# Kernel tuning notes

Measured on AMD Instinct MI355X. Metric: run time of the kernel, lower is better.

The kernel has to match this reference:

```python
import jax, jax.numpy as jnp
import numpy as np

B, C, H, W = 4, 256, 64, 64
GROUPS = 32
EPS = 1e-6
N_BITS_QKV = 8
N_BITS_SM = 8


def setup_inputs() -> dict:
    key = jax.random.key(0)
    ks = jax.random.split(key, 6)
    s = 1.0 / np.sqrt(C)
    return {
        "x": jax.random.normal(ks[0], (B, C, H, W), jnp.float32),
        "gn_scale": jnp.ones((C,), jnp.float32),
        "gn_bias": jnp.zeros((C,), jnp.float32),
        "wq": jax.random.normal(ks[1], (C, C), jnp.float32) * s,
        "bq": jnp.zeros((C,), jnp.float32),
        "wk": jax.random.normal(ks[2], (C, C), jnp.float32) * s,
        "bk": jnp.zeros((C,), jnp.float32),
        "wv": jax.random.normal(ks[3], (C, C), jnp.float32) * s,
        "bv": jnp.zeros((C,), jnp.float32),
        "wproj": jax.random.normal(ks[4], (C, C), jnp.float32) * s,
        "bproj": jnp.zeros((C,), jnp.float32),
        # per-tensor uniform-affine quantizer params (delta, zero_point)
        "dq": jnp.float32(8.0 / 255.0), "zq": jnp.float32(128.0),
        "dk": jnp.float32(8.0 / 255.0), "zk": jnp.float32(128.0),
        "dv": jnp.float32(8.0 / 255.0), "zv": jnp.float32(128.0),
        "dw": jnp.float32(1.0 / 255.0), "zw": jnp.float32(0.0),
    }


def ste_round(x):
    # round with straight-through gradient (as in round_ste of BRECQ/QDrop)
    return x + jax.lax.stop_gradient(jnp.round(x) - x)


def fake_quant(x, delta, zero_point, n_bits):
    # UniformAffineQuantizer: quant -> clamp -> dequant
    n_levels = 2 ** n_bits
    x_int = ste_round(x / delta) + zero_point
    x_q = jnp.clip(x_int, 0, n_levels - 1)
    return (x_q - zero_point) * delta


def group_norm(x, scale, bias):
    b, c, h, w = x.shape
    xg = x.reshape(b, GROUPS, (c // GROUPS) * h * w)
    mu = xg.mean(-1, keepdims=True)
    var = xg.var(-1, keepdims=True)
    xn = ((xg - mu) * jax.lax.rsqrt(var + EPS)).reshape(b, c, h, w)
    return xn * scale[None, :, None, None] + bias[None, :, None, None]


def conv1x1(x, w, b):
    # 1x1 conv == channel-mixing matmul
    return jnp.einsum('bchw,oc->bohw', x, w) + b[None, :, None, None]


def reference(x, gn_scale, gn_bias, wq, bq, wk, bk, wv, bv, wproj, bproj,
              dq, zq, dk, zk, dv, zv, dw, zw):
    h_ = group_norm(x, gn_scale, gn_bias)
    q = conv1x1(h_, wq, bq)
    k = conv1x1(h_, wk, bk)
    v = conv1x1(h_, wv, bv)
    b, c, h, w = q.shape
    hw = h * w
    q = q.reshape(b, c, hw).transpose(0, 2, 1)   # [b, hw, c]
    k = k.reshape(b, c, hw)                      # [b, c, hw]
    q = fake_quant(q, dq, zq, N_BITS_QKV)
    k = fake_quant(k, dk, zk, N_BITS_QKV)
    attn = jnp.einsum('bnc,bcm->bnm', q, k) * (c ** -0.5)  # [b, hw, hw]
    attn = jax.nn.softmax(attn, axis=2)
    v = fake_quant(v.reshape(b, c, hw), dv, zv, N_BITS_QKV)
    attn = fake_quant(attn.transpose(0, 2, 1), dw, zw, N_BITS_SM)  # [b, m, n]
    h_out = jnp.einsum('bcm,bmn->bcn', v, attn).reshape(b, c, h, w)
    return x + conv1x1(h_out, wproj, bproj)
```

## Files before the change

kernel.cpp:

```cpp
#include <hip/hip_runtime.h>


#define Bb 4
#define Cc 256
#define Nn 4096
#define NGRP 32
#define LOG2E 1.4426950408889634f

typedef unsigned short u16;
typedef unsigned int   u32;
typedef unsigned char  u8;
typedef __attribute__((ext_vector_type(8))) short bf16x8;
typedef __attribute__((ext_vector_type(4))) float f32x4;
typedef __attribute__((ext_vector_type(4))) int   i32x4;

#define MFMA16(a,b,c)    __builtin_amdgcn_mfma_f32_16x16x32_bf16((a),(b),(c),0,0,0)
#define MFMA_I8(a,b,c)   __builtin_amdgcn_mfma_i32_16x16x64_i8((a),(b),(c),0,0,0)
#define EXP2F(x)         __builtin_amdgcn_exp2f(x)

static __device__ __forceinline__ u16 f2bf(float x){
  u32 u = __float_as_uint(x);
  u += 0x7fffu + ((u >> 16) & 1u);
  return (u16)(u >> 16);
}
static __device__ __forceinline__ float bf2f(u16 h){ return __uint_as_float(((u32)h) << 16); }

union U64c { u16 u[4]; uint2 v; };

__global__ __launch_bounds__(256) void k_gn_stats(const float* __restrict__ x,
                                                  float* __restrict__ mu, float* __restrict__ rs){
  int bg = blockIdx.x;
  const float4* p = (const float4*)(x + (size_t)bg * (8 * Nn));
  float s = 0.f, q = 0.f;
  for (int i = threadIdx.x; i < 8*Nn/4; i += 256){
    float4 v = p[i];
    s += v.x + v.y + v.z + v.w;
    q += v.x*v.x + v.y*v.y + v.z*v.z + v.w*v.w;
  }
  __shared__ float rsum[256], rsq[256];
  rsum[threadIdx.x] = s; rsq[threadIdx.x] = q;
  __syncthreads();
  for (int off = 128; off > 0; off >>= 1){
    if (threadIdx.x < off){ rsum[threadIdx.x] += rsum[threadIdx.x+off]; rsq[threadIdx.x] += rsq[threadIdx.x+off]; }
    __syncthreads();
  }
  if (threadIdx.x == 0){
    const float inv = 1.0f / (8*Nn);
    float m = rsum[0]*inv;
    float var = rsq[0]*inv - m*m;
    mu[bg] = m; rs[bg] = rsqrtf(var + 1e-6f);
  }
}

__global__ __launch_bounds__(256) void k_wsplit(const float* __restrict__ wq, const float* __restrict__ wk,
                                                const float* __restrict__ wv, const float* __restrict__ wp,
                                                u16* __restrict__ WH, u16* __restrict__ WL){
  int gid = blockIdx.x*256 + threadIdx.x;
  int mat = gid >> 16, idx = gid & 65535;
  const float* src = (mat == 0) ? wq : (mat == 1) ? wk : (mat == 2) ? wv : wp;
  float w = src[idx];
  u16 h = f2bf(w);
  WH[gid] = h;
  WL[gid] = f2bf(w - bf2f(h));
}

__global__ __launch_bounds__(256) void k_gn_apply(const float* __restrict__ x,
                                                  const float* __restrict__ gsc, const float* __restrict__ gbi,
                                                  const float* __restrict__ mu, const float* __restrict__ rs,
                                                  u16* __restrict__ hhi, u16* __restrict__ hlo){
  int nt = blockIdx.x, ct = blockIdx.y, b = blockIdx.z;
  int n0 = nt*64, c0 = ct*64;
  __shared__ float yt[64*65];
  __shared__ float sa[64], sb[64];
  int t = threadIdx.x;
  if (t < 64){
    int c = c0 + t;
    int bg = b*NGRP + (c >> 3);
    float a = rs[bg] * gsc[c];
    sa[t] = a;
    sb[t] = gbi[c] - mu[bg]*a;
  }
  __syncthreads();
  #pragma unroll
  for (int j = 0; j < 4; ++j){
    int id = t + j*256;
    int r = id >> 4, cq = id & 15;
    float4 v = *(const float4*)(x + ((size_t)b*Cc + c0 + r)*Nn + n0 + cq*4);
    float a = sa[r], bb = sb[r];
    yt[r*65 + cq*4 + 0] = v.x*a + bb;
    yt[r*65 + cq*4 + 1] = v.y*a + bb;
    yt[r*65 + cq*4 + 2] = v.z*a + bb;
    yt[r*65 + cq*4 + 3] = v.w*a + bb;
  }
  __syncthreads();
  int nl = t >> 2, cg = (t & 3) * 16;
  size_t base = ((size_t)b*Nn + n0 + nl)*Cc + c0 + cg;
  #pragma unroll
  for (int half = 0; half < 2; ++half){
    union { u16 u[8]; uint4 v; } Ph, Pl;
    #pragma unroll
    for (int u = 0; u < 8; ++u){
      float y = yt[(cg + half*8 + u)*65 + nl];
      u16 h = f2bf(y);
      Ph.u[u] = h; Pl.u[u] = f2bf(y - bf2f(h));
    }
    *(uint4*)(hhi + base + half*8) = Ph.v;
    *(uint4*)(hlo + base + half*8) = Pl.v;
  }
}

__global__ __launch_bounds__(1024) void k_convqkv(const u16* __restrict__ WH, const u16* __restrict__ WL,
                                                 const u16* __restrict__ Hhi, const u16* __restrict__ Hlo,
                                                 const float* __restrict__ bq, const float* __restrict__ bk,
                                                 const float* __restrict__ bv,
                                                 const float* __restrict__ dq, const float* __restrict__ zq,
                                                 const float* __restrict__ dk, const float* __restrict__ zk,
                                                 const float* __restrict__ dv, const float* __restrict__ zv,
                                                 u8* __restrict__ qT8, u8* __restrict__ kT8,
                                                 u8* __restrict__ v8){
  int nt = blockIdx.x, b = blockIdx.y;
  __shared__ u16 Lh[64*256], Ll[64*256];
  int t = threadIdx.x, lane = t & 63, wave = t >> 6;
  int lo16 = lane & 15, quad = lane >> 4;
  int o0 = wave*16;

  {
    const u16* hb = Hhi + ((size_t)b*Nn + nt*64) * 256;
    const u16* lb = Hlo + ((size_t)b*Nn + nt*64) * 256;
    #pragma unroll
    for (int j = 0; j < 2; ++j){
      int id = t + j*1024;
      int r = id >> 5, ch = id & 31;
      int sw = (ch ^ (r & 15)) * 8;
      *(uint4*)(Lh + r*256 + sw) = *(const uint4*)(hb + (size_t)r*256 + ch*8);
      *(uint4*)(Ll + r*256 + sw) = *(const uint4*)(lb + (size_t)r*256 + ch*8);
    }
  }
  __syncthreads();

  const float* Bs[3] = {bq, bk, bv};
  const float* Dsr[3] = {dq, dk, dv};
  const float* Zs[3] = {zq, zk, zv};

  #pragma unroll
  for (int ws = 0; ws < 3; ++ws){
    bf16x8 awh[8], awl[8];
    {
      const u16* wbh = WH + (size_t)ws*65536 + (size_t)(o0 + lo16) * 256 + quad*8;
      const u16* wbl = WL + (size_t)ws*65536 + (size_t)(o0 + lo16) * 256 + quad*8;
      #pragma unroll
      for (int k = 0; k < 8; ++k){
        awh[k] = *(const bf16x8*)(wbh + k*32);
        awl[k] = *(const bf16x8*)(wbl + k*32);
      }
    }
    f32x4 zf = {0.f,0.f,0.f,0.f};
    f32x4 acc[4] = {zf, zf, zf, zf};
    #pragma unroll
    for (int k = 0; k < 8; ++k){
      #pragma unroll
      for (int ns = 0; ns < 4; ++ns){
        int r = ns*16 + lo16;
        int ph = ((k*4 + quad) ^ (r & 15)) * 8;
        bf16x8 bh = *(const bf16x8*)(Lh + r*256 + ph);
        bf16x8 bl = *(const bf16x8*)(Ll + r*256 + ph);
        acc[ns] = MFMA16(awh[k], bh, acc[ns]);
        acc[ns] = MFMA16(awl[k], bh, acc[ns]);
        acc[ns] = MFMA16(awh[k], bl, acc[ns]);
      }
    }
    float bia[4];
    #pragma unroll
    for (int r = 0; r < 4; ++r) bia[r] = Bs[ws][o0 + quad*4 + r];
    float z = Zs[ws][0]; float invd = 1.0f / Dsr[ws][0];

    if (ws < 2){
      u8* outT = (ws == 0) ? qT8 : kT8;
      #pragma unroll
      for (int ns = 0; ns < 4; ++ns){
        int n = nt*64 + ns*16 + lo16;
        u32 w = 0;
        #pragma unroll
        for (int r = 0; r < 4; ++r){
          float v = acc[ns][r] + bia[r];
          float xq = fminf(fmaxf(rintf(v*invd) + z, 0.f), 255.f);
          int qi = (int)rintf(xq - z);
          w |= ((u32)(qi & 255)) << (8*r);
        }
        *(u32*)(outT + ((size_t)b*Nn + n)*Cc + o0 + quad*4) = w;
      }
    } else {
      #pragma unroll
      for (int ns = 0; ns < 4; ++ns){
        int n = nt*64 + ns*16 + lo16;
        #pragma unroll
        for (int r = 0; r < 4; ++r){
          float v = acc[ns][r] + bia[r];
          float xq = fminf(fmaxf(rintf(v*invd) + z, 0.f), 255.f);
          int qi = (int)rintf(xq - z);
          v8[((size_t)b*Cc + o0 + quad*4 + r)*Nn + n] = (u8)(qi & 255);
        }
      }
    }
  }
}

static __device__ __forceinline__ int sq4(u32 w){
  int s = 0;
  #pragma unroll
  for (int j = 0; j < 4; ++j){ int v = (int)((signed char)((w >> (8*j)) & 0xffu)); s += v*v; }
  return s;
}
static __device__ __forceinline__ int ssum4(u32 w){
  return ((int)(w << 24) >> 24) + ((int)(w << 16) >> 24) + ((int)(w << 8) >> 24) + ((int)w >> 24);
}
__global__ __launch_bounds__(256) void k_normvs(const u8* __restrict__ qT8, const u8* __restrict__ kT8,
                                                const u8* __restrict__ v8,
                                                u32* __restrict__ stat, int* __restrict__ vsum){
  if (blockIdx.x < 128){
    int gid = blockIdx.x*256 + threadIdx.x;
    int which = gid >> 14;
    int rid = gid & 16383;
    const u8* row = (which ? kT8 : qT8) + (size_t)rid * 256;
    u32 acc = 0;
    const uint4* p = (const uint4*)row;
    #pragma unroll
    for (int i = 0; i < 16; ++i){
      uint4 w = p[i];
      acc += (u32)(sq4(w.x) + sq4(w.y) + sq4(w.z) + sq4(w.w));
    }
    #pragma unroll
    for (int msk = 32; msk > 0; msk >>= 1){
      u32 o = (u32)__shfl_xor((int)acc, msk, 64);
      acc = acc > o ? acc : o;
    }
    if ((threadIdx.x & 63) == 0)
      atomicMax(&stat[which*4 + (rid >> 12)], acc);
  } else {
    int row = blockIdx.x - 128;
    uint4 w = *(const uint4*)(v8 + (size_t)row*Nn + threadIdx.x*16);
    int s = ssum4(w.x) + ssum4(w.y) + ssum4(w.z) + ssum4(w.w);
    #pragma unroll
    for (int msk = 1; msk < 64; msk <<= 1) s += __shfl_xor(s, msk, 64);
    __shared__ int r4[4];
    if ((threadIdx.x & 63) == 0) r4[threadIdx.x >> 6] = s;
    __syncthreads();
    if (threadIdx.x == 0) vsum[row] = r4[0] + r4[1] + r4[2] + r4[3];
  }
}

__global__ __launch_bounds__(1024) void k_qpv(const u8* __restrict__ qT8, const u8* __restrict__ kT8,
                                              const u8* __restrict__ v8,
                                              const u32* __restrict__ stat,
                                              const float* __restrict__ pdq, const float* __restrict__ pdk,
                                              const float* __restrict__ pdw, const float* __restrict__ pzw,
                                              const int* __restrict__ vsum,
                                              const float* __restrict__ pdv,
                                              const u16* __restrict__ WH, const u16* __restrict__ WL,
                                              const float* __restrict__ bp,
                                              const float* __restrict__ xres,
                                              float* __restrict__ outF){
  int nt = blockIdx.x, b = blockIdx.y;
  __shared__ alignas(16) u8  Kt[2][2][64*256];
  __shared__ alignas(16) u32 Pt[2][2][64*16];
  __shared__ float Lbuf[4][4][16];
  int t = threadIdx.x, lane = t & 63, w = t >> 6;
  int lo16 = lane & 15, q = lane >> 4;
  int ms = w & 3, nsq = w >> 2;

  float sc2 = pdq[0]*pdk[0]*0.0625f*LOG2E;
  float M2 = sc2 * sqrtf((float)stat[b] * (float)stat[4+b]);
  float zw = pzw[0];

  i32x4 qf[4];
  {
    const u8* qb = qT8 + ((size_t)b*Nn + nt*64 + nsq*16 + lo16)*256;
    #pragma unroll
    for (int kk = 0; kk < 4; ++kk)
      qf[kk] = *(const i32x4*)(qb + kk*64 + q*16);
  }

  int krow = t >> 4, kch = t & 15;
  int kdst = krow*256 + ((kch ^ (krow & 15)) << 4);
  const u8* kb = kT8 + (size_t)b*Nn*256;

  int mrow = ms*16 + lo16;
  int kofs[4];
  #pragma unroll
  for (int kk = 0; kk < 4; ++kk) kofs[kk] = mrow*256 + (((kk*4 + q) ^ (mrow & 15)) << 4);

  const u8* vp = v8 + ((size_t)(b*Cc + w*16 + lo16))*Nn + q*16;

  float lr = 0.f;
  {
    const u8* kld = kb + (size_t)krow*256 + kch*16;
    uint4 kr0 = *(const uint4*)(kld);
    uint4 kr1 = *(const uint4*)(kld + 16384);
    *(uint4*)(Kt[0][0] + kdst) = kr0;
    *(uint4*)(Kt[0][1] + kdst) = kr1;
    kld += 2*16384;
    kr0 = *(const uint4*)(kld);
    kr1 = *(const uint4*)(kld + 16384);
    kld += 2*16384;
    __syncthreads();
    i32x4 spA0, spB0, spA1, spB1;
    #pragma unroll 2
    for (int i = 0; i < 32; ++i){
      int cur = i & 1;
      i32x4 sA0 = {0,0,0,0}, sB0 = {0,0,0,0}, sA1 = {0,0,0,0}, sB1 = {0,0,0,0};
      sA0 = MFMA_I8(*(const i32x4*)(Kt[cur][0] + kofs[0]), qf[0], sA0);
      sB0 = MFMA_I8(*(const i32x4*)(Kt[cur][0] + kofs[1]), qf[1], sB0);
      sA1 = MFMA_I8(*(const i32x4*)(Kt[cur][1] + kofs[0]), qf[0], sA1);
      sB1 = MFMA_I8(*(const i32x4*)(Kt[cur][1] + kofs[1]), qf[1], sB1);
      sA0 = MFMA_I8(*(const i32x4*)(Kt[cur][0] + kofs[2]), qf[2], sA0);
      sB0 = MFMA_I8(*(const i32x4*)(Kt[cur][0] + kofs[3]), qf[3], sB0);
      sA1 = MFMA_I8(*(const i32x4*)(Kt[cur][1] + kofs[2]), qf[2], sA1);
      sB1 = MFMA_I8(*(const i32x4*)(Kt[cur][1] + kofs[3]), qf[3], sB1);
      if (i < 31){
        *(uint4*)(Kt[cur ^ 1][0] + kdst) = kr0;
        *(uint4*)(Kt[cur ^ 1][1] + kdst) = kr1;
        if (i < 30){
          kr0 = *(const uint4*)(kld);
          kr1 = *(const uint4*)(kld + 16384);
          kld += 2*16384;
        }
      }
      if (i > 0){
        #pragma unroll
        for (int r = 0; r < 4; ++r){
          lr += EXP2F(fmaf((float)(spA0[r] + spB0[r]), sc2, -M2));
          lr += EXP2F(fmaf((float)(spA1[r] + spB1[r]), sc2, -M2));
        }
      }
      spA0 = sA0; spB0 = sB0; spA1 = sA1; spB1 = sB1;
      __syncthreads();
    }
    #pragma unroll
    for (int r = 0; r < 4; ++r){
      lr += EXP2F(fmaf((float)(spA0[r] + spB0[r]), sc2, -M2));
      lr += EXP2F(fmaf((float)(spA1[r] + spB1[r]), sc2, -M2));
    }
  }
  lr += __shfl_xor(lr, 16, 64);
  lr += __shfl_xor(lr, 32, 64);
  if (lane < 16) Lbuf[nsq][ms][lo16] = lr;
  __syncthreads();
  float Ls = Lbuf[nsq][0][lo16] + Lbuf[nsq][1][lo16] + Lbuf[nsq][2][lo16] + Lbuf[nsq][3][lo16];
  float crn = __log2f(1.0f / (pdw[0] * Ls)) - M2;

  i32x4 zi = {0,0,0,0};
  i32x4 acc[4] = {zi,zi,zi,zi};
  int nrow = nsq*16 + lo16;
  int pdst = nrow*16 + ((ms ^ (nrow & 3) ^ ((nrow >> 2) & 3)) << 2) + q;
  int pofs[4];
  #pragma unroll
  for (int ns = 0; ns < 4; ++ns){
    int pr = ns*16 + lo16;
    pofs[ns] = pr*16 + ((q ^ (pr & 3) ^ ((pr >> 2) & 3)) << 2);
  }
  {
    const u8* kld = kb + (size_t)krow*256 + kch*16;
    uint4 kr0 = *(const uint4*)(kld);
    uint4 kr1 = *(const uint4*)(kld + 16384);
    *(uint4*)(Kt[0][0] + kdst) = kr0;
    *(uint4*)(Kt[0][1] + kdst) = kr1;
    kld += 2*16384;
    kr0 = *(const uint4*)(kld);
    kr1 = *(const uint4*)(kld + 16384);
    kld += 2*16384;
    const u8* vld = vp + 128;
    i32x4 af0 = *(const i32x4*)(vp);
    i32x4 af1 = *(const i32x4*)(vp + 64);
    i32x4 af0p, af1p, af0pp, af1pp;
    i32x4 spA0, spB0, spA1, spB1;
    __syncthreads();
    #pragma unroll 2
    for (int i = 0; i < 32; ++i){
      int cur = i & 1;
      i32x4 sA0 = {0,0,0,0}, sB0 = {0,0,0,0}, sA1 = {0,0,0,0}, sB1 = {0,0,0,0};
      sA0 = MFMA_I8(*(const i32x4*)(Kt[cur][0] + kofs[0]), qf[0], sA0);
      sB0 = MFMA_I8(*(const i32x4*)(Kt[cur][0] + kofs[1]), qf[1], sB0);
      sA1 = MFMA_I8(*(const i32x4*)(Kt[cur][1] + kofs[0]), qf[0], sA1);
      sB1 = MFMA_I8(*(const i32x4*)(Kt[cur][1] + kofs[1]), qf[1], sB1);
      sA0 = MFMA_I8(*(const i32x4*)(Kt[cur][0] + kofs[2]), qf[2], sA0);
      sB0 = MFMA_I8(*(const i32x4*)(Kt[cur][0] + kofs[3]), qf[3], sB0);
      sA1 = MFMA_I8(*(const i32x4*)(Kt[cur][1] + kofs[2]), qf[2], sA1);
      sB1 = MFMA_I8(*(const i32x4*)(Kt[cur][1] + kofs[3]), qf[3], sB1);
      if (i < 31){
        *(uint4*)(Kt[cur ^ 1][0] + kdst) = kr0;
        *(uint4*)(Kt[cur ^ 1][1] + kdst) = kr1;
        if (i < 30){
          kr0 = *(const uint4*)(kld);
          kr1 = *(const uint4*)(kld + 16384);
          kld += 2*16384;
        }
      }
      if (i > 1){
        acc[0] = MFMA_I8(af0pp, *(const i32x4*)(Pt[cur][0] + pofs[0]), acc[0]);
        acc[1] = MFMA_I8(af0pp, *(const i32x4*)(Pt[cur][0] + pofs[1]), acc[1]);
        acc[2] = MFMA_I8(af0pp, *(const i32x4*)(Pt[cur][0] + pofs[2]), acc[2]);
        acc[3] = MFMA_I8(af0pp, *(const i32x4*)(Pt[cur][0] + pofs[3]), acc[3]);
        acc[0] = MFMA_I8(af1pp, *(const i32x4*)(Pt[cur][1] + pofs[0]), acc[0]);
        acc[1] = MFMA_I8(af1pp, *(const i32x4*)(Pt[cur][1] + pofs[1]), acc[1]);
        acc[2] = MFMA_I8(af1pp, *(const i32x4*)(Pt[cur][1] + pofs[2]), acc[2]);
        acc[3] = MFMA_I8(af1pp, *(const i32x4*)(Pt[cur][1] + pofs[3]), acc[3]);
      }
      if (i > 0){
        u32 wp0 = 0, wp1 = 0;
        #pragma unroll
        for (int r = 0; r < 4; ++r){
          float at0 = EXP2F(fmaf((float)(spA0[r] + spB0[r]), sc2, crn));
          float y0 = fminf(fmaxf(rintf(at0) + zw, 0.f), 255.f);
          wp0 = __builtin_amdgcn_cvt_pk_u8_f32(y0, (u32)r, wp0);
          float at1 = EXP2F(fmaf((float)(spA1[r] + spB1[r]), sc2, crn));
          float y1 = fminf(fmaxf(rintf(at1) + zw, 0.f), 255.f);
          wp1 = __builtin_amdgcn_cvt_pk_u8_f32(y1, (u32)r, wp1);
        }
        Pt[cur ^ 1][0][pdst] = wp0 ^ 0x80808080u;
        Pt[cur ^ 1][1][pdst] = wp1 ^ 0x80808080u;
      }
      spA0 = sA0; spB0 = sB0; spA1 = sA1; spB1 = sB1;
      af0pp = af0p; af0p = af0; af1pp = af1p; af1p = af1;
      if (i < 31){
        af0 = *(const i32x4*)(vld);
        af1 = *(const i32x4*)(vld + 64);
        vld += 128;
      }
      __syncthreads();
    }
    acc[0] = MFMA_I8(af0pp, *(const i32x4*)(Pt[0][0] + pofs[0]), acc[0]);
    acc[1] = MFMA_I8(af0pp, *(const i32x4*)(Pt[0][0] + pofs[1]), acc[1]);
    acc[2] = MFMA_I8(af0pp, *(const i32x4*)(Pt[0][0] + pofs[2]), acc[2]);
    acc[3] = MFMA_I8(af0pp, *(const i32x4*)(Pt[0][0] + pofs[3]), acc[3]);
    acc[0] = MFMA_I8(af1pp, *(const i32x4*)(Pt[0][1] + pofs[0]), acc[0]);
    acc[1] = MFMA_I8(af1pp, *(const i32x4*)(Pt[0][1] + pofs[1]), acc[1]);
    acc[2] = MFMA_I8(af1pp, *(const i32x4*)(Pt[0][1] + pofs[2]), acc[2]);
    acc[3] = MFMA_I8(af1pp, *(const i32x4*)(Pt[0][1] + pofs[3]), acc[3]);
    {
      u32 wp0 = 0, wp1 = 0;
      #pragma unroll
      for (int r = 0; r < 4; ++r){
        float at0 = EXP2F(fmaf((float)(spA0[r] + spB0[r]), sc2, crn));
        float y0 = fminf(fmaxf(rintf(at0) + zw, 0.f), 255.f);
        wp0 = __builtin_amdgcn_cvt_pk_u8_f32(y0, (u32)r, wp0);
        float at1 = EXP2F(fmaf((float)(spA1[r] + spB1[r]), sc2, crn));
        float y1 = fminf(fmaxf(rintf(at1) + zw, 0.f), 255.f);
        wp1 = __builtin_amdgcn_cvt_pk_u8_f32(y1, (u32)r, wp1);
      }
      Pt[1][0][pdst] = wp0 ^ 0x80808080u;
      Pt[1][1][pdst] = wp1 ^ 0x80808080u;
    }
    __syncthreads();
    acc[0] = MFMA_I8(af0p, *(const i32x4*)(Pt[1][0] + pofs[0]), acc[0]);
    acc[1] = MFMA_I8(af0p, *(const i32x4*)(Pt[1][0] + pofs[1]), acc[1]);
    acc[2] = MFMA_I8(af0p, *(const i32x4*)(Pt[1][0] + pofs[2]), acc[2]);
    acc[3] = MFMA_I8(af0p, *(const i32x4*)(Pt[1][0] + pofs[3]), acc[3]);
    acc[0] = MFMA_I8(af1p, *(const i32x4*)(Pt[1][1] + pofs[0]), acc[0]);
    acc[1] = MFMA_I8(af1p, *(const i32x4*)(Pt[1][1] + pofs[1]), acc[1]);
    acc[2] = MFMA_I8(af1p, *(const i32x4*)(Pt[1][1] + pofs[2]), acc[2]);
    acc[3] = MFMA_I8(af1p, *(const i32x4*)(Pt[1][1] + pofs[3]), acc[3]);
  }

  u16* Ht = (u16*)Kt;
  {
    float s = pdv[0] * pdw[0];
    float corr = s * (128.0f - zw);
    int c0 = w*16 + q*4;
    int kc0 = c0 >> 7;
    int ch8 = (c0 >> 3) & 15;
    int c4  = c0 & 7;
    float cv[4];
    #pragma unroll
    for (int r = 0; r < 4; ++r) cv[r] = corr * (float)vsum[b*Cc + c0 + r];
    #pragma unroll
    for (int ns = 0; ns < 4; ++ns){
      int rrow = ns*16 + lo16;
      U64c Uh;
      #pragma unroll
      for (int r = 0; r < 4; ++r)
        Uh.u[r] = f2bf(s*(float)acc[ns][r] + cv[r]);
      *(uint2*)(Ht + rrow*256 + kc0*128 + ((ch8 ^ (rrow & 7)) << 3) + c4) = Uh.v;
    }
  }
  __syncthreads();
  {
    f32x4 zf = {0.f,0.f,0.f,0.f};
    f32x4 acc2[4] = {zf, zf, zf, zf};
    const u16* wbh = WH + (size_t)3*65536 + (size_t)(w*16 + lo16)*256 + q*8;
    const u16* wbl = WL + (size_t)3*65536 + (size_t)(w*16 + lo16)*256 + q*8;
    #pragma unroll
    for (int kc = 0; kc < 2; ++kc){
      bf16x8 ah[4], al[4];
      #pragma unroll
      for (int k4 = 0; k4 < 4; ++k4){
        ah[k4] = *(const bf16x8*)(wbh + kc*128 + k4*32);
        al[k4] = *(const bf16x8*)(wbl + kc*128 + k4*32);
      }
      #pragma unroll
      for (int k4 = 0; k4 < 4; ++k4){
        #pragma unroll
        for (int ns = 0; ns < 4; ++ns){
          int rrow = ns*16 + lo16;
          bf16x8 bh = *(const bf16x8*)(Ht + rrow*256 + kc*128 + (((k4*4 + q) ^ (rrow & 7)) << 3));
          acc2[ns] = MFMA16(ah[k4], bh, acc2[ns]);
          acc2[ns] = MFMA16(al[k4], bh, acc2[ns]);
        }
      }
    }
    float bia[4];
    #pragma unroll
    for (int r = 0; r < 4; ++r) bia[r] = bp[w*16 + q*4 + r];
    #pragma unroll
    for (int ns = 0; ns < 4; ++ns){
      int n = nt*64 + ns*16 + lo16;
      #pragma unroll
      for (int r = 0; r < 4; ++r){
        size_t a = ((size_t)b*Cc + w*16 + q*4 + r)*Nn + n;
        outF[a] = xres[a] + acc2[ns][r] + bia[r];
      }
    }
  }
}

extern "C" void kernel_launch(void* const* d_in, const int* in_sizes, int n_in,
                              void* d_out, int out_size, void* d_ws, size_t ws_size,
                              hipStream_t stream){
  (void)in_sizes; (void)n_in; (void)out_size; (void)ws_size;
  const float* x   = (const float*)d_in[0];
  const float* gsc = (const float*)d_in[1];
  const float* gbi = (const float*)d_in[2];
  const float* wq  = (const float*)d_in[3];
  const float* bq  = (const float*)d_in[4];
  const float* wk  = (const float*)d_in[5];
  const float* bk  = (const float*)d_in[6];
  const float* wv  = (const float*)d_in[7];
  const float* bv  = (const float*)d_in[8];
  const float* wp  = (const float*)d_in[9];
  const float* bp  = (const float*)d_in[10];
  const float* dq  = (const float*)d_in[11];
  const float* zq  = (const float*)d_in[12];
  const float* dk  = (const float*)d_in[13];
  const float* zk  = (const float*)d_in[14];
  const float* dv  = (const float*)d_in[15];
  const float* zv  = (const float*)d_in[16];
  const float* dw  = (const float*)d_in[17];
  const float* zw  = (const float*)d_in[18];
  float* out = (float*)d_out;

  const size_t SZT = (size_t)Bb*Nn*Cc;
  u16* hT_hi = (u16*)d_ws;
  u16* hT_lo = hT_hi + SZT;
  u16* h2    = hT_lo + SZT;
  u8*  qT8   = (u8*)(h2 + SZT);
  u8*  kT8   = qT8 + SZT;
  u8*  v8    = kT8 + SZT;
  u16* WH    = (u16*)(v8 + SZT);
  u16* WL    = WH + 4*65536;
  float* mu  = (float*)(WL + 4*65536);
  float* rs  = mu + 128;
  u32*  stat = (u32*)(rs + 128);
  int*  vsum = (int*)(stat + 8);

  k_gn_stats<<<dim3(Bb*NGRP), 256, 0, stream>>>(x, mu, rs);
  k_wsplit<<<dim3(1024), 256, 0, stream>>>(wq, wk, wv, wp, WH, WL);
  k_gn_apply<<<dim3(Nn/64, Cc/64, Bb), 256, 0, stream>>>(x, gsc, gbi, mu, rs, hT_hi, hT_lo);

  k_convqkv<<<dim3(Nn/64, Bb), 1024, 0, stream>>>(WH, WL, hT_hi, hT_lo,
                                                  bq, bk, bv, dq, zq, dk, zk, dv, zv,
                                                  qT8, kT8, v8);

  hipMemsetAsync(stat, 0, 8*sizeof(u32), stream);
  k_normvs<<<dim3(128 + Bb*Cc), 256, 0, stream>>>(qT8, kT8, v8, stat, vsum);

  k_qpv<<<dim3(Nn/64, Bb), 1024, 0, stream>>>(qT8, kT8, v8, stat, dq, dk, dw, zw, vsum, dv,
                                              WH, WL, bp, x, out);
}
```

Before: 244.3 us.

## Fuse group-norm apply and norm/vsum statistics into QKV conv kernel

The group-norm application moves into the QKV 1x1-conv kernel. Each block now reads x directly, normalizes it, splits it into bf16 hi/lo parts and writes those into swizzled LDS, so the hT_hi/hT_lo global intermediates are no longer written and read back. The per-row squared-norm max statistics for q/k and the per-channel v sums are computed in the conv epilogue through LDS and global atomics, which removes the separate k_normvs pass that re-read the int8 outputs. In exchange the conv kernel needs more LDS and extra barriers in a serialized four-step staging loop, and it adds atomic contention.

```diff
diff --git a/kernel.cpp b/kernel.cpp
--- a/kernel.cpp
+++ b/kernel.cpp
@@ -64,79 +64,66 @@
   WL[gid] = f2bf(w - bf2f(h));
 }
 
-__global__ __launch_bounds__(256) void k_gn_apply(const float* __restrict__ x,
-                                                  const float* __restrict__ gsc, const float* __restrict__ gbi,
-                                                  const float* __restrict__ mu, const float* __restrict__ rs,
-                                                  u16* __restrict__ hhi, u16* __restrict__ hlo){
-  int nt = blockIdx.x, ct = blockIdx.y, b = blockIdx.z;
-  int n0 = nt*64, c0 = ct*64;
-  __shared__ float yt[64*65];
-  __shared__ float sa[64], sb[64];
-  int t = threadIdx.x;
-  if (t < 64){
-    int c = c0 + t;
-    int bg = b*NGRP + (c >> 3);
-    float a = rs[bg] * gsc[c];
-    sa[t] = a;
-    sb[t] = gbi[c] - mu[bg]*a;
-  }
-  __syncthreads();
-  #pragma unroll
-  for (int j = 0; j < 4; ++j){
-    int id = t + j*256;
-    int r = id >> 4, cq = id & 15;
-    float4 v = *(const float4*)(x + ((size_t)b*Cc + c0 + r)*Nn + n0 + cq*4);
-    float a = sa[r], bb = sb[r];
-    yt[r*65 + cq*4 + 0] = v.x*a + bb;
-    yt[r*65 + cq*4 + 1] = v.y*a + bb;
-    yt[r*65 + cq*4 + 2] = v.z*a + bb;
-    yt[r*65 + cq*4 + 3] = v.w*a + bb;
-  }
-  __syncthreads();
-  int nl = t >> 2, cg = (t & 3) * 16;
-  size_t base = ((size_t)b*Nn + n0 + nl)*Cc + c0 + cg;
-  #pragma unroll
-  for (int half = 0; half < 2; ++half){
-    union { u16 u[8]; uint4 v; } Ph, Pl;
-    #pragma unroll
-    for (int u = 0; u < 8; ++u){
-      float y = yt[(cg + half*8 + u)*65 + nl];
-      u16 h = f2bf(y);
-      Ph.u[u] = h; Pl.u[u] = f2bf(y - bf2f(h));
-    }
-    *(uint4*)(hhi + base + half*8) = Ph.v;
-    *(uint4*)(hlo + base + half*8) = Pl.v;
-  }
-}
-
-__global__ __launch_bounds__(1024) void k_convqkv(const u16* __restrict__ WH, const u16* __restrict__ WL,
-                                                 const u16* __restrict__ Hhi, const u16* __restrict__ Hlo,
+__global__ __launch_bounds__(1024) void k_convqkv(const float* __restrict__ x,
+                                                 const float* __restrict__ gsc, const float* __restrict__ gbi,
+                                                 const float* __restrict__ mu, const float* __restrict__ rs,
+                                                 const u16* __restrict__ WH, const u16* __restrict__ WL,
                                                  const float* __restrict__ bq, const float* __restrict__ bk,
                                                  const float* __restrict__ bv,
                                                  const float* __restrict__ dq, const float* __restrict__ zq,
                                                  const float* __restrict__ dk, const float* __restrict__ zk,
                                                  const float* __restrict__ dv, const float* __restrict__ zv,
                                                  u8* __restrict__ qT8, u8* __restrict__ kT8,
-                                                 u8* __restrict__ v8){
+                                                 u8* __restrict__ v8,
+                                                 u32* __restrict__ stat, int* __restrict__ vsum){
   int nt = blockIdx.x, b = blockIdx.y;
   __shared__ u16 Lh[64*256], Ll[64*256];
+  __shared__ float yt[64*65];
+  __shared__ float sa[256], sb[256];
+  __shared__ u32 rowacc[2][64];
   int t = threadIdx.x, lane = t & 63, wave = t >> 6;
   int lo16 = lane & 15, quad = lane >> 4;
   int o0 = wave*16;
+  int n0 = nt*64;
+
+  if (t < 256){
+    int c = t;
+    int bg = b*NGRP + (c >> 3);
+    float a = rs[bg] * gsc[c];
+    sa[c] = a;
+    sb[c] = gbi[c] - mu[bg]*a;
+  }
+  if (t < 128) rowacc[t >> 6][t & 63] = 0;
+  __syncthreads();
 
   {
-    const u16* hb = Hhi + ((size_t)b*Nn + nt*64) * 256;
-    const u16* lb = Hlo + ((size_t)b*Nn + nt*64) * 256;
-    #pragma unroll
-    for (int j = 0; j < 2; ++j){
-      int id = t + j*1024;
-      int r = id >> 5, ch = id & 31;
-      int sw = (ch ^ (r & 15)) * 8;
-      *(uint4*)(Lh + r*256 + sw) = *(const uint4*)(hb + (size_t)r*256 + ch*8);
-      *(uint4*)(Ll + r*256 + sw) = *(const uint4*)(lb + (size_t)r*256 + ch*8);
-    }
-  }
-  __syncthreads();
+    int r  = t >> 4, cq = t & 15;
+    int nl = t >> 4, c4 = t & 15;
+    #pragma unroll
+    for (int ct = 0; ct < 4; ++ct){
+      int c0 = ct*64;
+      float4 xv = *(const float4*)(x + ((size_t)b*Cc + c0 + r)*Nn + n0 + cq*4);
+      float a = sa[c0 + r], bb = sb[c0 + r];
+      yt[r*65 + cq*4 + 0] = xv.x*a + bb;
+      yt[r*65 + cq*4 + 1] = xv.y*a + bb;
+      yt[r*65 + cq*4 + 2] = xv.z*a + bb;
+      yt[r*65 + cq*4 + 3] = xv.w*a + bb;
+      __syncthreads();
+      int cg = c0 + c4*4;
+      union { u16 us[4]; uint2 v2; } Ph, Pl;
+      #pragma unroll
+      for (int uu = 0; uu < 4; ++uu){
+        float y = yt[(c4*4 + uu)*65 + nl];
+        u16 h = f2bf(y);
+        Ph.us[uu] = h; Pl.us[uu] = f2bf(y - bf2f(h));
+      }
+      int ch = cg >> 3;
+      int addr = nl*256 + ((ch ^ (nl & 15)) << 3) + (cg & 7);
+      *(uint2*)(Lh + addr) = Ph.v2;
+      *(uint2*)(Ll + addr) = Pl.v2;
+      __syncthreads();
+    }
+  }
 
   const float* Bs[3] = {bq, bk, bv};
   const float* Dsr[3] = {dq, dk, dv};
@@ -179,17 +166,23 @@
       #pragma unroll
       for (int ns = 0; ns < 4; ++ns){
         int n = nt*64 + ns*16 + lo16;
-        u32 w = 0;
+        u32 wpk = 0;
+        int nrm = 0;
         #pragma unroll
         for (int r = 0; r < 4; ++r){
           float v = acc[ns][r] + bia[r];
           float xq = fminf(fmaxf(rintf(v*invd) + z, 0.f), 255.f);
           int qi = (int)rintf(xq - z);
-          w |= ((u32)(qi & 255)) << (8*r);
-        }
-        *(u32*)(outT + ((size_t)b*Nn + n)*Cc + o0 + quad*4) = w;
+          nrm += qi*qi;
+          wpk |= ((u32)(qi & 255)) << (8*r);
+        }
+        *(u32*)(outT + ((size_t)b*Nn + n)*Cc + o0 + quad*4) = wpk;
+        nrm += __shfl_xor(nrm, 16, 64);
+        nrm += __shfl_xor(nrm, 32, 64);
+        if (lane < 16) atomicAdd(&rowacc[ws][ns*16 + lo16], (u32)nrm);
       }
     } else {
+      int vpart[4] = {0, 0, 0, 0};
       #pragma unroll
       for (int ns = 0; ns < 4; ++ns){
         int n = nt*64 + ns*16 + lo16;
@@ -198,54 +191,33 @@
           float v = acc[ns][r] + bia[r];
           float xq = fminf(fmaxf(rintf(v*invd) + z, 0.f), 255.f);
           int qi = (int)rintf(xq - z);
+          vpart[r] += qi;
           v8[((size_t)b*Cc + o0 + quad*4 + r)*Nn + n] = (u8)(qi & 255);
         }
       }
-    }
-  }
-}
-
-static __device__ __forceinline__ int sq4(u32 w){
-  int s = 0;
-  #pragma unroll
-  for (int j = 0; j < 4; ++j){ int v = (int)((signed char)((w >> (8*j)) & 0xffu)); s += v*v; }
-  return s;
-}
-static __device__ __forceinline__ int ssum4(u32 w){
-  return ((int)(w << 24) >> 24) + ((int)(w << 16) >> 24) + ((int)(w << 8) >> 24) + ((int)w >> 24);
-}
-__global__ __launch_bounds__(256) void k_normvs(const u8* __restrict__ qT8, const u8* __restrict__ kT8,
-                                                const u8* __restrict__ v8,
-                                                u32* __restrict__ stat, int* __restrict__ vsum){
-  if (blockIdx.x < 128){
-    int gid = blockIdx.x*256 + threadIdx.x;
-    int which = gid >> 14;
-    int rid = gid & 16383;
-    const u8* row = (which ? kT8 : qT8) + (size_t)rid * 256;
-    u32 acc = 0;
-    const uint4* p = (const uint4*)row;
-    #pragma unroll
-    for (int i = 0; i < 16; ++i){
-      uint4 w = p[i];
-      acc += (u32)(sq4(w.x) + sq4(w.y) + sq4(w.z) + sq4(w.w));
-    }
-    #pragma unroll
-    for (int msk = 32; msk > 0; msk >>= 1){
-      u32 o = (u32)__shfl_xor((int)acc, msk, 64);
-      acc = acc > o ? acc : o;
-    }
-    if ((threadIdx.x & 63) == 0)
-      atomicMax(&stat[which*4 + (rid >> 12)], acc);
-  } else {
-    int row = blockIdx.x - 128;
-    uint4 w = *(const uint4*)(v8 + (size_t)row*Nn + threadIdx.x*16);
-    int s = ssum4(w.x) + ssum4(w.y) + ssum4(w.z) + ssum4(w.w);
-    #pragma unroll
-    for (int msk = 1; msk < 64; msk <<= 1) s += __shfl_xor(s, msk, 64);
-    __shared__ int r4[4];
-    if ((threadIdx.x & 63) == 0) r4[threadIdx.x >> 6] = s;
-    __syncthreads();
-    if (threadIdx.x == 0) vsum[row] = r4[0] + r4[1] + r4[2] + r4[3];
+      #pragma unroll
+      for (int r = 0; r < 4; ++r){
+        #pragma unroll
+        for (int m = 1; m < 16; m <<= 1)
+          vpart[r] += __shfl_xor(vpart[r], m, 64);
+      }
+      if (lo16 == 0){
+        #pragma unroll
+        for (int r = 0; r < 4; ++r)
+          atomicAdd(&vsum[b*Cc + o0 + quad*4 + r], vpart[r]);
+      }
+    }
+  }
+
+  __syncthreads();
+  if (wave < 2){
+    u32 v = rowacc[wave][lane];
+    #pragma unroll
+    for (int m = 1; m < 64; m <<= 1){
+      u32 o = (u32)__shfl_xor((int)v, m, 64);
+      v = v > o ? v : o;
+    }
+    if (lane == 0) atomicMax(&stat[wave*4 + b], v);
   }
 }
 
@@ -563,14 +535,11 @@
 
   k_gn_stats<<<dim3(Bb*NGRP), 256, 0, stream>>>(x, mu, rs);
   k_wsplit<<<dim3(1024), 256, 0, stream>>>(wq, wk, wv, wp, WH, WL);
-  k_gn_apply<<<dim3(Nn/64, Cc/64, Bb), 256, 0, stream>>>(x, gsc, gbi, mu, rs, hT_hi, hT_lo);
-
-  k_convqkv<<<dim3(Nn/64, Bb), 1024, 0, stream>>>(WH, WL, hT_hi, hT_lo,
+  hipMemsetAsync(stat, 0, (8 + Bb*Cc)*sizeof(u32), stream);
+
+  k_convqkv<<<dim3(Nn/64, Bb), 1024, 0, stream>>>(x, gsc, gbi, mu, rs, WH, WL,
                                                   bq, bk, bv, dq, zq, dk, zk, dv, zv,
-                                                  qT8, kT8, v8);
-
-  hipMemsetAsync(stat, 0, 8*sizeof(u32), stream);
-  k_normvs<<<dim3(128 + Bb*Cc), 256, 0, stream>>>(qT8, kT8, v8, stat, vsum);
+                                                  qT8, kT8, v8, stat, vsum);
 
   k_qpv<<<dim3(Nn/64, Bb), 1024, 0, stream>>>(qT8, kT8, v8, stat, dq, dk, dw, zw, vsum, dv,
                                               WH, WL, bp, x, out);
```

After: 240.8 us. No clear change (-1.4%).
